# Optimization experiments

Hardware: AMD Instinct MI355X
Metric: run time of the kernel (lower is better)

The kernel has to match this reference:

```python
import jax, jax.numpy as jnp
import numpy as np

B, S, H, E = 4, 2048, 1024, 8


def setup_inputs() -> dict:
    key = jax.random.key(0)
    k1, k2, k3 = jax.random.split(key, 3)
    scale = 1.0 / np.sqrt(H)
    return {
        "x": jax.random.normal(k1, (B, S, H), dtype=jnp.float32),
        "router_w": jax.random.normal(k2, (H, E), dtype=jnp.float32) * scale,
        "router_b": jnp.zeros((E,), dtype=jnp.float32),
        "expert_w": jax.random.normal(k3, (E, H, H), dtype=jnp.float32) * scale,
        "expert_b": jnp.zeros((E, H), dtype=jnp.float32),
    }


def reference(x, router_w, router_b, expert_w, expert_b):
    # Flatten tokens: [T, H]
    b, s, h = x.shape
    hs = x.reshape(-1, h)
    # Router: logits -> softmax -> top-1 expert (argmax), matching the
    # original forward which routes each token to argmax(softmax(logits)).
    logits = hs @ router_w + router_b                 # [T, E]
    probs = jax.nn.softmax(logits, axis=-1)           # [T, E]
    idx = jnp.argmax(probs, axis=-1)                  # [T]
    gate = jnp.take_along_axis(probs, idx[:, None], axis=-1)  # [T, 1]
    # Per-expert GEMM computed densely for all experts (reference baseline
    # for the sort/dispatch + grouped-GEMM kernel): [T, E, H]
    expert_out = jnp.einsum("th,ehd->ted", hs, expert_w) + expert_b
    # Combine: select routed expert's output, weight by gate value.
    dispatch = jax.nn.one_hot(idx, expert_w.shape[0], dtype=hs.dtype) * gate  # [T, E]
    out = jnp.einsum("te,ted->td", dispatch, expert_out)  # [T, H]
    return out.reshape(b, s, h)
```

## Files before the change

### kernel.cpp

```cpp
#include <hip/hip_runtime.h>

constexpr int kT = 8192;
constexpr int kH = 1024;
constexpr int kE = 8;
constexpr int kMaxRows  = 9216;
constexpr int kMaxTiles = 72;
constexpr int kNS  = 8;
constexpr int kSeg = kH / kNS;
constexpr int kCntStride = 32;

typedef short short8 __attribute__((ext_vector_type(8)));
typedef float floatx4 __attribute__((ext_vector_type(4)));

__device__ inline unsigned short f2b(float f) {
    union { float f; unsigned int u; } v; v.f = f;
    unsigned int r = v.u + 0x7FFFu + ((v.u >> 16) & 1u);
    return (unsigned short)(r >> 16);
}

#define GLDS16(gp, lp)                                                                  \
    __builtin_amdgcn_global_load_lds(                                                   \
        (const __attribute__((address_space(1))) unsigned int*)(gp),                    \
        (__attribute__((address_space(3))) unsigned int*)(lp), 16, 0, 0)

__global__ __launch_bounds__(256) void k_prep(const float* __restrict__ W,
                                              unsigned short* __restrict__ Wt,
                                              const float* __restrict__ x,
                                              const float* __restrict__ rw,
                                              float* __restrict__ plog,
                                              int* __restrict__ cnt,
                                              int* __restrict__ done) {
    __shared__ float lds[64][65];
    int bid = blockIdx.x;
    int tid = threadIdx.x;
    if (bid == 0 && tid < kE + 1) {
        if (tid < kE) cnt[tid * kCntStride] = 0; else *done = 0;
    }
    if (bid < 2048) {
        int kb = bid & 15, nb = (bid >> 4) & 15, e = bid >> 8;
        int rr = tid >> 4, c4 = tid & 15;
        const float* Wp = W + ((size_t)e << 20) + (size_t)(kb * 64) * kH + nb * 64;
#pragma unroll
        for (int p = 0; p < 4; ++p) {
            int r = p * 16 + rr;
            float4 v = *(const float4*)(Wp + (size_t)r * kH + c4 * 4);
            lds[r][c4 * 4 + 0] = v.x; lds[r][c4 * 4 + 1] = v.y;
            lds[r][c4 * 4 + 2] = v.z; lds[r][c4 * 4 + 3] = v.w;
        }
        __syncthreads();
        unsigned short* Wo = Wt + ((size_t)e << 20) + (size_t)(nb * 64) * kH + kb * 64;
#pragma unroll
        for (int p = 0; p < 4; ++p) {
            int n = p * 16 + rr;
            ushort4 o;
            o.x = f2b(lds[c4 * 4 + 0][n]);
            o.y = f2b(lds[c4 * 4 + 1][n]);
            o.z = f2b(lds[c4 * 4 + 2][n]);
            o.w = f2b(lds[c4 * 4 + 3][n]);
            *(ushort4*)(Wo + (size_t)n * kH + c4 * 4) = o;
        }
    } else {
        int rb = bid - 2048;
        int seg = rb >> 8;
        int wave = (rb & 255) * 4 + (tid >> 6);
        int lane = tid & 63;
        int tg = lane >> 3, e = lane & 7;
        int t = wave * 8 + tg;
        const float* xp = x + (size_t)t * kH + seg * kSeg;
        const float* wp = rw + (size_t)seg * kSeg * kE + e;
        float a0 = 0.f, a1 = 0.f;
#pragma unroll 4
        for (int i = 0; i < kSeg / 8; ++i) {
            float4 v0 = *(const float4*)(xp + i * 8);
            float4 v1 = *(const float4*)(xp + i * 8 + 4);
            a0 += v0.x * wp[(i * 8 + 0) * kE];
            a0 += v0.y * wp[(i * 8 + 1) * kE];
            a0 += v0.z * wp[(i * 8 + 2) * kE];
            a0 += v0.w * wp[(i * 8 + 3) * kE];
            a1 += v1.x * wp[(i * 8 + 4) * kE];
            a1 += v1.y * wp[(i * 8 + 5) * kE];
            a1 += v1.z * wp[(i * 8 + 6) * kE];
            a1 += v1.w * wp[(i * 8 + 7) * kE];
        }
        plog[(size_t)t * 64 + e * 8 + seg] = a0 + a1;
    }
}

__global__ __launch_bounds__(256) void k_router_final(const float* __restrict__ plog,
                                                      const float* __restrict__ rb,
                                                      int* __restrict__ idx, float* __restrict__ gate,
                                                      int* __restrict__ rank, int* __restrict__ cnt,
                                                      int* __restrict__ done,
                                                      int* __restrict__ aoff,
                                                      int* __restrict__ tile_e,
                                                      int* __restrict__ tile_row) {
    __shared__ int lcnt[kE];
    __shared__ int lbase[kE];
    int tid = threadIdx.x;
    if (tid < kE) lcnt[tid] = 0;
    __syncthreads();

    int wave = blockIdx.x * 4 + (tid >> 6);
    int lane = tid & 63;
    int tg = lane >> 3, e = lane & 7;
    int t = wave * 8 + tg;
    const float* pp = plog + (size_t)t * 64 + e * 8;
    float4 p0 = *(const float4*)pp;
    float4 p1 = *(const float4*)(pp + 4);
    float acc = rb[e] + ((p0.x + p0.y) + (p0.z + p0.w)) + ((p1.x + p1.y) + (p1.z + p1.w));
    float m = acc; int bi = e;
#pragma unroll
    for (int s = 1; s < 8; s <<= 1) {
        float om = __shfl_xor(m, s);
        int   ob = __shfl_xor(bi, s);
        if (om > m || (om == m && ob < bi)) { m = om; bi = ob; }
    }
    float p = __expf(acc - m);
    float sum = p;
#pragma unroll
    for (int s = 1; s < 8; s <<= 1) sum += __shfl_xor(sum, s);

    int lrank = 0;
    if (e == 0) {
        idx[t]  = bi;
        gate[t] = 1.0f / sum;
        lrank = atomicAdd(&lcnt[bi], 1);
    }
    __syncthreads();
    if (tid < kE) lbase[tid] = atomicAdd(&cnt[tid * kCntStride], lcnt[tid]);
    __syncthreads();
    if (e == 0) rank[t] = lbase[bi] + lrank;

    __syncthreads();
    if (tid == 0) {
        __threadfence();
        int old = atomicAdd(done, 1);
        if (old == (int)gridDim.x - 1) {
            __threadfence();
            int off = 0, tt = 0;
            for (int ee = 0; ee < kE; ++ee) {
                aoff[ee] = off;
                int c = atomicAdd(&cnt[ee * kCntStride], 0);
                int nt = (c + 127) >> 7;
                for (int i = 0; i < nt; ++i) { tile_e[tt] = ee; tile_row[tt] = off + (i << 7); ++tt; }
                off += nt << 7;
            }
            aoff[kE] = off;
            for (; tt < kMaxTiles; ++tt) tile_e[tt] = -1;
        }
    }
}

__global__ __launch_bounds__(256) void k_gather(const float* __restrict__ x,
                                                const float* __restrict__ gate,
                                                const int* __restrict__ idx,
                                                const int* __restrict__ rank,
                                                const int* __restrict__ aoff,
                                                const int* __restrict__ cnt,
                                                int* __restrict__ perm,
                                                float* __restrict__ grow,
                                                unsigned short* __restrict__ A) {
    int bid = blockIdx.x;
    int c = threadIdx.x;
    if (bid < kT) {
        int t = bid;
        int e = idx[t];
        int row = aoff[e] + rank[t];
        const float* xp = x + (size_t)t * kH;
        float4 v = *(const float4*)(xp + c * 4);
        ushort4 o; o.x = f2b(v.x); o.y = f2b(v.y); o.z = f2b(v.z); o.w = f2b(v.w);
        *(ushort4*)(A + (size_t)row * kH + c * 4) = o;
        if (c == 0) { perm[row] = t; grow[row] = gate[t]; }
    } else {
        int r = bid - kT;
        if (r >= aoff[kE]) return;
        int e = 0;
        while (r >= aoff[e + 1]) ++e;
        if (r - aoff[e] < cnt[e * kCntStride]) return;
        ushort4 z; z.x = 0; z.y = 0; z.z = 0; z.w = 0;
        *(ushort4*)(A + (size_t)r * kH + c * 4) = z;
        if (c == 0) perm[r] = -1;
    }
}

constexpr int kBK = 64;

__global__ __launch_bounds__(256, 2) void k_gemm(const unsigned short* __restrict__ A,
                                                 const unsigned short* __restrict__ Wt,
                                                 const float* __restrict__ eb,
                                                 const int* __restrict__ perm,
                                                 const float* __restrict__ grow,
                                                 const int* __restrict__ tile_e,
                                                 const int* __restrict__ tile_row,
                                                 float* __restrict__ out) {
    int bm = blockIdx.x, bn = blockIdx.y;
    int e = tile_e[bm];
    if (e < 0) return;
    int rowbase = tile_row[bm];

    __shared__ __align__(16) unsigned short As[128 * kBK];
    __shared__ __align__(16) unsigned short Bs[128 * kBK];

    int tid = threadIdx.x;
    int wave = tid >> 6, lane = tid & 63;
    int wm = wave & 1, wn = wave >> 1;
    int quad = lane >> 4, l15 = lane & 15;

    floatx4 acc[4][4];
#pragma unroll
    for (int i = 0; i < 4; ++i)
#pragma unroll
        for (int j = 0; j < 4; ++j) acc[i][j] = floatx4{0.f, 0.f, 0.f, 0.f};

    const unsigned short* Ab = A + (size_t)rowbase * kH;
    const unsigned short* Bb = Wt + ((size_t)e << 20) + (size_t)(bn * 128) * kH;

    int lrow8 = lane >> 3;
    int lseg8 = (lane & 7) ^ lrow8;
    const unsigned short* aP = Ab + (size_t)(wave * 32 + lrow8) * kH + lseg8 * 8;
    const unsigned short* bP = Bb + (size_t)(wave * 32 + lrow8) * kH + lseg8 * 8;
    unsigned short* lA = &As[(wave * 32) * kBK];
    unsigned short* lB = &Bs[(wave * 32) * kBK];

    int sw0 = ((0 * 4 + quad) ^ (l15 & 7)) * 8;
    int sw1 = ((1 * 4 + quad) ^ (l15 & 7)) * 8;

    for (int k0 = 0; k0 < kH; k0 += kBK) {
        __syncthreads();
#pragma unroll
        for (int j = 0; j < 4; ++j) {
            GLDS16(aP + (size_t)(j * 8) * kH + k0, lA + j * 8 * kBK);
            GLDS16(bP + (size_t)(j * 8) * kH + k0, lB + j * 8 * kBK);
        }
        __syncthreads();

        short8 af[4][2], bf[4][2];
#pragma unroll
        for (int i = 0; i < 4; ++i) {
            int r = (wm * 64 + i * 16 + l15) * kBK;
            af[i][0] = *(const short8*)&As[r + sw0];
            af[i][1] = *(const short8*)&As[r + sw1];
        }
#pragma unroll
        for (int i = 0; i < 4; ++i) {
            int r = (wn * 64 + i * 16 + l15) * kBK;
            bf[i][0] = *(const short8*)&Bs[r + sw0];
            bf[i][1] = *(const short8*)&Bs[r + sw1];
        }
#pragma unroll
        for (int ks = 0; ks < 2; ++ks)
#pragma unroll
            for (int i = 0; i < 4; ++i)
#pragma unroll
                for (int j = 0; j < 4; ++j)
                    acc[i][j] = __builtin_amdgcn_mfma_f32_16x16x32_bf16(af[i][ks], bf[j][ks],
                                                                        acc[i][j], 0, 0, 0);
    }

    int colbase = bn * 128 + wn * 64;
#pragma unroll
    for (int i = 0; i < 4; ++i) {
        int rl = rowbase + wm * 64 + i * 16 + quad * 4;
#pragma unroll
        for (int rg = 0; rg < 4; ++rg) {
            int r = rl + rg;
            int tok = perm[r];
            if (tok < 0) continue;
            float g = grow[r];
            float* op = out + (size_t)tok * kH;
#pragma unroll
            for (int j = 0; j < 4; ++j) {
                int col = colbase + j * 16 + l15;
                op[col] = g * (acc[i][j][rg] + eb[e * kH + col]);
            }
        }
    }
}

extern "C" void kernel_launch(void* const* d_in, const int* in_sizes, int n_in,
                              void* d_out, int out_size, void* d_ws, size_t ws_size,
                              hipStream_t stream) {
    const float* x  = (const float*)d_in[0];
    const float* rw = (const float*)d_in[1];
    const float* rb = (const float*)d_in[2];
    const float* ew = (const float*)d_in[3];
    const float* eb = (const float*)d_in[4];
    float* out = (float*)d_out;

    char* p = (char*)d_ws;
    unsigned short* Wt = (unsigned short*)p; p += (size_t)kE * kH * kH * 2;
    unsigned short* A  = (unsigned short*)p; p += (size_t)kMaxRows * kH * 2;
    float* plog = (float*)p; p += (size_t)kT * 64 * 4;
    float* gate = (float*)p; p += (size_t)kT * 4;
    float* grow = (float*)p; p += (size_t)kMaxRows * 4;
    int* idx    = (int*)p;   p += (size_t)kT * 4;
    int* rank   = (int*)p;   p += (size_t)kT * 4;
    int* perm   = (int*)p;   p += (size_t)kMaxRows * 4;
    int* cnt    = (int*)p;   p += kE * kCntStride * 4;
    int* aoff   = (int*)p;   p += 64;
    int* done   = (int*)p;   p += 64;
    int* tile_e = (int*)p;   p += kMaxTiles * 4;
    int* tile_r = (int*)p;   p += kMaxTiles * 4;

    k_prep<<<4096, 256, 0, stream>>>(ew, Wt, x, rw, plog, cnt, done);
    k_router_final<<<kT / 32, 256, 0, stream>>>(plog, rb, idx, gate, rank, cnt, done,
                                                aoff, tile_e, tile_r);
    k_gather<<<kT + kMaxRows, 256, 0, stream>>>(x, gate, idx, rank, aoff, cnt, perm, grow, A);
    dim3 gg(kMaxTiles, kH / 128);
    k_gemm<<<gg, 256, 0, stream>>>(A, Wt, eb, perm, grow, tile_e, tile_r, out);
}
```

Measured before the change: 184.2 us.

## Drop gather kernel; GEMM loads token rows indirectly from bf16-converted x

Removes the separate gather/pad kernel. x is now converted to bf16 in place inside the prep kernel, and the router writes per-expert token lists. The GEMM then fetches A rows by token index through per-lane pointers and masks padded rows using the expert count. The router partial-logit blocks also stage router weights transposed in LDS for vectorized reads. This saves one kernel launch and the scattered A write/read, at the cost of non-contiguous row loads in the GEMM.

```diff
diff --git a/kernel.cpp b/kernel.cpp
--- a/kernel.cpp
+++ b/kernel.cpp
@@ -3,7 +3,6 @@
 constexpr int kT = 8192;
 constexpr int kH = 1024;
 constexpr int kE = 8;
-constexpr int kMaxRows  = 9216;
 constexpr int kMaxTiles = 72;
 constexpr int kNS  = 8;
 constexpr int kSeg = kH / kNS;
@@ -26,17 +25,19 @@
 __global__ __launch_bounds__(256) void k_prep(const float* __restrict__ W,
                                               unsigned short* __restrict__ Wt,
                                               const float* __restrict__ x,
+                                              unsigned short* __restrict__ xb,
                                               const float* __restrict__ rw,
                                               float* __restrict__ plog,
                                               int* __restrict__ cnt,
                                               int* __restrict__ done) {
-    __shared__ float lds[64][65];
+    __shared__ __align__(16) char smem[16640];
     int bid = blockIdx.x;
     int tid = threadIdx.x;
     if (bid == 0 && tid < kE + 1) {
         if (tid < kE) cnt[tid * kCntStride] = 0; else *done = 0;
     }
     if (bid < 2048) {
+        float (*lds)[65] = (float(*)[65])smem;
         int kb = bid & 15, nb = (bid >> 4) & 15, e = bid >> 8;
         int rr = tid >> 4, c4 = tid & 15;
         const float* Wp = W + ((size_t)e << 20) + (size_t)(kb * 64) * kH + nb * 64;
@@ -59,28 +60,43 @@
             o.w = f2b(lds[c4 * 4 + 3][n]);
             *(ushort4*)(Wo + (size_t)n * kH + c4 * 4) = o;
         }
+    } else if (bid < 6144) {
+        int row = (bid - 2048) * 2 + (tid >> 7);
+        int col = (tid & 127) * 8;
+        const float* xp = x + (size_t)row * kH + col;
+        float4 v0 = *(const float4*)xp;
+        float4 v1 = *(const float4*)(xp + 4);
+        ushort4 o0, o1;
+        o0.x = f2b(v0.x); o0.y = f2b(v0.y); o0.z = f2b(v0.z); o0.w = f2b(v0.w);
+        o1.x = f2b(v1.x); o1.y = f2b(v1.y); o1.z = f2b(v1.z); o1.w = f2b(v1.w);
+        unsigned short* op = xb + (size_t)row * kH + col;
+        *(ushort4*)op = o0;
+        *(ushort4*)(op + 4) = o1;
     } else {
-        int rb = bid - 2048;
-        int seg = rb >> 8;
-        int wave = (rb & 255) * 4 + (tid >> 6);
+        float (*rwT)[132] = (float(*)[132])smem;
+        int rbk = bid - 6144;
+        int seg = rbk >> 8;
+        {
+            int hl = tid >> 1, ep = (tid & 1) * 4;
+            float4 v = *(const float4*)(rw + (size_t)(seg * kSeg + hl) * kE + ep);
+            rwT[ep + 0][hl] = v.x; rwT[ep + 1][hl] = v.y;
+            rwT[ep + 2][hl] = v.z; rwT[ep + 3][hl] = v.w;
+        }
+        __syncthreads();
+        int wave = (rbk & 255) * 4 + (tid >> 6);
         int lane = tid & 63;
         int tg = lane >> 3, e = lane & 7;
         int t = wave * 8 + tg;
         const float* xp = x + (size_t)t * kH + seg * kSeg;
-        const float* wp = rw + (size_t)seg * kSeg * kE + e;
         float a0 = 0.f, a1 = 0.f;
 #pragma unroll 4
         for (int i = 0; i < kSeg / 8; ++i) {
-            float4 v0 = *(const float4*)(xp + i * 8);
-            float4 v1 = *(const float4*)(xp + i * 8 + 4);
-            a0 += v0.x * wp[(i * 8 + 0) * kE];
-            a0 += v0.y * wp[(i * 8 + 1) * kE];
-            a0 += v0.z * wp[(i * 8 + 2) * kE];
-            a0 += v0.w * wp[(i * 8 + 3) * kE];
-            a1 += v1.x * wp[(i * 8 + 4) * kE];
-            a1 += v1.y * wp[(i * 8 + 5) * kE];
-            a1 += v1.z * wp[(i * 8 + 6) * kE];
-            a1 += v1.w * wp[(i * 8 + 7) * kE];
+            float4 xv0 = *(const float4*)(xp + i * 8);
+            float4 xv1 = *(const float4*)(xp + i * 8 + 4);
+            float4 wv0 = *(const float4*)&rwT[e][i * 8];
+            float4 wv1 = *(const float4*)&rwT[e][i * 8 + 4];
+            a0 += xv0.x * wv0.x + xv0.y * wv0.y + xv0.z * wv0.z + xv0.w * wv0.w;
+            a1 += xv1.x * wv1.x + xv1.y * wv1.y + xv1.z * wv1.z + xv1.w * wv1.w;
         }
         plog[(size_t)t * 64 + e * 8 + seg] = a0 + a1;
     }
@@ -88,10 +104,10 @@
 
 __global__ __launch_bounds__(256) void k_router_final(const float* __restrict__ plog,
                                                       const float* __restrict__ rb,
-                                                      int* __restrict__ idx, float* __restrict__ gate,
-                                                      int* __restrict__ rank, int* __restrict__ cnt,
+                                                      float* __restrict__ gate,
+                                                      int* __restrict__ perm2,
+                                                      int* __restrict__ cnt,
                                                       int* __restrict__ done,
-                                                      int* __restrict__ aoff,
                                                       int* __restrict__ tile_e,
                                                       int* __restrict__ tile_row) {
     __shared__ int lcnt[kE];
@@ -122,14 +138,13 @@
 
     int lrank = 0;
     if (e == 0) {
-        idx[t]  = bi;
         gate[t] = 1.0f / sum;
         lrank = atomicAdd(&lcnt[bi], 1);
     }
     __syncthreads();
     if (tid < kE) lbase[tid] = atomicAdd(&cnt[tid * kCntStride], lcnt[tid]);
     __syncthreads();
-    if (e == 0) rank[t] = lbase[bi] + lrank;
+    if (e == 0) perm2[bi * kT + lbase[bi] + lrank] = t;
 
     __syncthreads();
     if (tid == 0) {
@@ -137,66 +152,34 @@
         int old = atomicAdd(done, 1);
         if (old == (int)gridDim.x - 1) {
             __threadfence();
-            int off = 0, tt = 0;
+            int tt = 0;
             for (int ee = 0; ee < kE; ++ee) {
-                aoff[ee] = off;
                 int c = atomicAdd(&cnt[ee * kCntStride], 0);
                 int nt = (c + 127) >> 7;
-                for (int i = 0; i < nt; ++i) { tile_e[tt] = ee; tile_row[tt] = off + (i << 7); ++tt; }
-                off += nt << 7;
+                for (int i = 0; i < nt; ++i) { tile_e[tt] = ee; tile_row[tt] = i << 7; ++tt; }
             }
-            aoff[kE] = off;
             for (; tt < kMaxTiles; ++tt) tile_e[tt] = -1;
         }
     }
 }
 
-__global__ __launch_bounds__(256) void k_gather(const float* __restrict__ x,
-                                                const float* __restrict__ gate,
-                                                const int* __restrict__ idx,
-                                                const int* __restrict__ rank,
-                                                const int* __restrict__ aoff,
-                                                const int* __restrict__ cnt,
-                                                int* __restrict__ perm,
-                                                float* __restrict__ grow,
-                                                unsigned short* __restrict__ A) {
-    int bid = blockIdx.x;
-    int c = threadIdx.x;
-    if (bid < kT) {
-        int t = bid;
-        int e = idx[t];
-        int row = aoff[e] + rank[t];
-        const float* xp = x + (size_t)t * kH;
-        float4 v = *(const float4*)(xp + c * 4);
-        ushort4 o; o.x = f2b(v.x); o.y = f2b(v.y); o.z = f2b(v.z); o.w = f2b(v.w);
-        *(ushort4*)(A + (size_t)row * kH + c * 4) = o;
-        if (c == 0) { perm[row] = t; grow[row] = gate[t]; }
-    } else {
-        int r = bid - kT;
-        if (r >= aoff[kE]) return;
-        int e = 0;
-        while (r >= aoff[e + 1]) ++e;
-        if (r - aoff[e] < cnt[e * kCntStride]) return;
-        ushort4 z; z.x = 0; z.y = 0; z.z = 0; z.w = 0;
-        *(ushort4*)(A + (size_t)r * kH + c * 4) = z;
-        if (c == 0) perm[r] = -1;
-    }
-}
-
 constexpr int kBK = 64;
 
-__global__ __launch_bounds__(256, 2) void k_gemm(const unsigned short* __restrict__ A,
+__global__ __launch_bounds__(256, 2) void k_gemm(const unsigned short* __restrict__ xb,
                                                  const unsigned short* __restrict__ Wt,
                                                  const float* __restrict__ eb,
-                                                 const int* __restrict__ perm,
-                                                 const float* __restrict__ grow,
+                                                 const int* __restrict__ perm2,
+                                                 const float* __restrict__ gate,
+                                                 const int* __restrict__ cnt,
                                                  const int* __restrict__ tile_e,
                                                  const int* __restrict__ tile_row,
                                                  float* __restrict__ out) {
     int bm = blockIdx.x, bn = blockIdx.y;
     int e = tile_e[bm];
     if (e < 0) return;
-    int rowbase = tile_row[bm];
+    int l0 = tile_row[bm];
+    int ce = cnt[e * kCntStride];
+    const int* pe = perm2 + e * kT;
 
     __shared__ __align__(16) unsigned short As[128 * kBK];
     __shared__ __align__(16) unsigned short Bs[128 * kBK];
@@ -212,13 +195,17 @@
 #pragma unroll
         for (int j = 0; j < 4; ++j) acc[i][j] = floatx4{0.f, 0.f, 0.f, 0.f};
 
-    const unsigned short* Ab = A + (size_t)rowbase * kH;
-    const unsigned short* Bb = Wt + ((size_t)e << 20) + (size_t)(bn * 128) * kH;
-
     int lrow8 = lane >> 3;
     int lseg8 = (lane & 7) ^ lrow8;
-    const unsigned short* aP = Ab + (size_t)(wave * 32 + lrow8) * kH + lseg8 * 8;
-    const unsigned short* bP = Bb + (size_t)(wave * 32 + lrow8) * kH + lseg8 * 8;
+    const unsigned short* aPj[4];
+#pragma unroll
+    for (int j = 0; j < 4; ++j) {
+        int lr = l0 + wave * 32 + j * 8 + lrow8;
+        int tok = (lr < ce) ? pe[lr] : 0;
+        aPj[j] = xb + (size_t)tok * kH + lseg8 * 8;
+    }
+    const unsigned short* bP = Wt + ((size_t)e << 20)
+                             + (size_t)(bn * 128 + wave * 32 + lrow8) * kH + lseg8 * 8;
     unsigned short* lA = &As[(wave * 32) * kBK];
     unsigned short* lB = &Bs[(wave * 32) * kBK];
 
@@ -229,7 +216,7 @@
         __syncthreads();
 #pragma unroll
         for (int j = 0; j < 4; ++j) {
-            GLDS16(aP + (size_t)(j * 8) * kH + k0, lA + j * 8 * kBK);
+            GLDS16(aPj[j] + k0, lA + j * 8 * kBK);
             GLDS16(bP + (size_t)(j * 8) * kH + k0, lB + j * 8 * kBK);
         }
         __syncthreads();
@@ -260,13 +247,13 @@
     int colbase = bn * 128 + wn * 64;
 #pragma unroll
     for (int i = 0; i < 4; ++i) {
-        int rl = rowbase + wm * 64 + i * 16 + quad * 4;
+        int rl = l0 + wm * 64 + i * 16 + quad * 4;
 #pragma unroll
         for (int rg = 0; rg < 4; ++rg) {
-            int r = rl + rg;
-            int tok = perm[r];
-            if (tok < 0) continue;
-            float g = grow[r];
+            int lr = rl + rg;
+            if (lr >= ce) continue;
+            int tok = pe[lr];
+            float g = gate[tok];
             float* op = out + (size_t)tok * kH;
 #pragma unroll
             for (int j = 0; j < 4; ++j) {
@@ -289,23 +276,18 @@
 
     char* p = (char*)d_ws;
     unsigned short* Wt = (unsigned short*)p; p += (size_t)kE * kH * kH * 2;
-    unsigned short* A  = (unsigned short*)p; p += (size_t)kMaxRows * kH * 2;
-    float* plog = (float*)p; p += (size_t)kT * 64 * 4;
-    float* gate = (float*)p; p += (size_t)kT * 4;
-    float* grow = (float*)p; p += (size_t)kMaxRows * 4;
-    int* idx    = (int*)p;   p += (size_t)kT * 4;
-    int* rank   = (int*)p;   p += (size_t)kT * 4;
-    int* perm   = (int*)p;   p += (size_t)kMaxRows * 4;
-    int* cnt    = (int*)p;   p += kE * kCntStride * 4;
-    int* aoff   = (int*)p;   p += 64;
-    int* done   = (int*)p;   p += 64;
-    int* tile_e = (int*)p;   p += kMaxTiles * 4;
-    int* tile_r = (int*)p;   p += kMaxTiles * 4;
-
-    k_prep<<<4096, 256, 0, stream>>>(ew, Wt, x, rw, plog, cnt, done);
-    k_router_final<<<kT / 32, 256, 0, stream>>>(plog, rb, idx, gate, rank, cnt, done,
-                                                aoff, tile_e, tile_r);
-    k_gather<<<kT + kMaxRows, 256, 0, stream>>>(x, gate, idx, rank, aoff, cnt, perm, grow, A);
+    unsigned short* xb = (unsigned short*)p; p += (size_t)kT * kH * 2;
+    float* plog  = (float*)p; p += (size_t)kT * 64 * 4;
+    float* gate  = (float*)p; p += (size_t)kT * 4;
+    int* perm2   = (int*)p;   p += (size_t)kE * kT * 4;
+    int* cnt     = (int*)p;   p += kE * kCntStride * 4;
+    int* done    = (int*)p;   p += 64;
+    int* tile_e  = (int*)p;   p += kMaxTiles * 4;
+    int* tile_r  = (int*)p;   p += kMaxTiles * 4;
+
+    k_prep<<<8192, 256, 0, stream>>>(ew, Wt, x, xb, rw, plog, cnt, done);
+    k_router_final<<<kT / 32, 256, 0, stream>>>(plog, rb, gate, perm2, cnt, done,
+                                                tile_e, tile_r);
     dim3 gg(kMaxTiles, kH / 128);
-    k_gemm<<<gg, 256, 0, stream>>>(A, Wt, eb, perm, grow, tile_e, tile_r, out);
-}
+    k_gemm<<<gg, 256, 0, stream>>>(xb, Wt, eb, perm2, gate, cnt, tile_e, tile_r, out);
+}
```

New measurement: 167.9 us. 1.1x faster.
